# Kernel tuning notes

Measured on AMD Instinct MI355X. Metric: run time of the kernel, lower is better.

The kernel has to match this reference:

```python
import jax, jax.numpy as jnp
import numpy as np

N_NODES = 50000


def setup_inputs() -> dict:
    key = jax.random.key(0)
    k1, k2, k3, k4, k5 = jax.random.split(key, 5)
    E = 1600000
    features = jax.random.normal(k1, (N_NODES, 256), dtype=jnp.float32)
    weight = jax.random.normal(k2, (256, 64), dtype=jnp.float32) * (1.0 / np.sqrt(256))
    edge_row = jax.random.randint(k3, (E,), 0, N_NODES, dtype=jnp.int64 if jax.config.jax_enable_x64 else jnp.int32)
    edge_col = jax.random.randint(k4, (E,), 0, N_NODES, dtype=jnp.int64 if jax.config.jax_enable_x64 else jnp.int32)
    edge_weight = jax.random.uniform(k5, (E,), dtype=jnp.float32)
    return {
        "features": features,
        "weight": weight,
        "edge_row": edge_row,
        "edge_col": edge_col,
        "edge_weight": edge_weight,
        "active": 1,
    }


def reference(features, weight, edge_row, edge_col, edge_weight, active):
    # support = features @ W  -- dense projection [N, out]
    support = features @ weight
    # output = spmm(adj, support): gather source rows, scale by edge weight,
    # scatter-add into destination rows (COO SpMM).
    msgs = support[edge_col] * edge_weight[:, None]           # [E, out]
    output = jax.ops.segment_sum(msgs, edge_row, num_segments=N_NODES)  # [N, out]
    if active:
        output = jnp.tanh(output)
    return output
```

## Files before the change

### kernel.cpp

```cpp
#include <hip/hip_runtime.h>
#include <hip/hip_fp16.h>
#include <math.h>

#define N_NODES 50000
#define IN_F 256
#define OUT_F 64
#define NBUCK 391
#define CHUNK 4096
#define CAPB 4608

typedef unsigned int uint;


__global__ __launch_bounds__(256) void gemm_kernel(const float* __restrict__ feat,
                                                   const float* __restrict__ W,
                                                   __half* __restrict__ sup,
                                                   int* __restrict__ gcnt) {
    if (blockIdx.x == 0) {
        for (int i = threadIdx.x; i < NBUCK; i += 256) gcnt[i] = 0;
    }

    __shared__ float A_s[128 * 18];
    __shared__ float B_s[16 * 64];

    const int t = threadIdx.x;
    const int row0 = blockIdx.x * 128;
    const int tc = t & 15;
    const int tr = t >> 4;
    const int ar = t >> 2;
    const int ac = t & 3;

    int gr0 = row0 + ar;      if (gr0 >= N_NODES) gr0 = N_NODES - 1;
    int gr1 = row0 + ar + 64; if (gr1 >= N_NODES) gr1 = N_NODES - 1;
    const float4* gA0 = (const float4*)(feat + (size_t)gr0 * IN_F);
    const float4* gA1 = (const float4*)(feat + (size_t)gr1 * IN_F);
    const float4* gB  = (const float4*)W;

    float acc[8][4];
#pragma unroll
    for (int r = 0; r < 8; ++r)
#pragma unroll
        for (int i = 0; i < 4; ++i) acc[r][i] = 0.f;

    float4 a0 = gA0[ac];
    float4 a1 = gA1[ac];
    float4 bb = gB[(t >> 4) * 16 + tc];

    for (int ch = 0; ch < 16; ++ch) {
        {
            float* ap0 = &A_s[ar * 18 + ac * 4];
            ap0[0] = a0.x; ap0[1] = a0.y; ap0[2] = a0.z; ap0[3] = a0.w;
            float* ap1 = &A_s[(ar + 64) * 18 + ac * 4];
            ap1[0] = a1.x; ap1[1] = a1.y; ap1[2] = a1.z; ap1[3] = a1.w;
            *(float4*)&B_s[(t >> 4) * 64 + tc * 4] = bb;
        }
        __syncthreads();

        if (ch < 15) {
            a0 = gA0[(ch + 1) * 4 + ac];
            a1 = gA1[(ch + 1) * 4 + ac];
            bb = gB[((ch + 1) * 16 + (t >> 4)) * 16 + tc];
        }

#pragma unroll
        for (int k = 0; k < 16; ++k) {
            float b0 = B_s[k * 64 + tc * 4 + 0];
            float b1 = B_s[k * 64 + tc * 4 + 1];
            float b2 = B_s[k * 64 + tc * 4 + 2];
            float b3 = B_s[k * 64 + tc * 4 + 3];
#pragma unroll
            for (int r = 0; r < 8; ++r) {
                float av = A_s[(tr * 8 + r) * 18 + k];
                acc[r][0] += av * b0;
                acc[r][1] += av * b1;
                acc[r][2] += av * b2;
                acc[r][3] += av * b3;
            }
        }
        __syncthreads();
    }

#pragma unroll
    for (int r = 0; r < 8; ++r) {
        int row = row0 + tr * 8 + r;
        if (row < N_NODES) {
            __half2 h01 = __floats2half2_rn(acc[r][0], acc[r][1]);
            __half2 h23 = __floats2half2_rn(acc[r][2], acc[r][3]);
            uint2 u;
            u.x = *(unsigned int*)&h01;
            u.y = *(unsigned int*)&h23;
            *(uint2*)&sup[(size_t)row * OUT_F + tc * 4] = u;
        }
    }
}

__global__ __launch_bounds__(1024) void bin_kernel(const int* __restrict__ erow,
                                                   const int* __restrict__ ecol,
                                                   const float* __restrict__ ew,
                                                   int* __restrict__ gcnt,
                                                   int2* __restrict__ ecw, int E) {
    __shared__ int   h[NBUCK];
    __shared__ uint  pkst[CHUNK];
    __shared__ float wst[CHUNK];
    const int t = threadIdx.x;
    const int base = blockIdx.x * CHUNK;

    for (int i = t; i < NBUCK; i += 1024) h[i] = 0;
    __syncthreads();

    const int e4 = base + 4 * t;
    if (e4 + 3 < E) {
        int4   r4 = *(const int4*)(erow + e4);
        int4   c4 = *(const int4*)(ecol + e4);
        float4 w4 = *(const float4*)(ew + e4);
        pkst[4 * t + 0] = ((uint)r4.x << 16) | (uint)c4.x;
        pkst[4 * t + 1] = ((uint)r4.y << 16) | (uint)c4.y;
        pkst[4 * t + 2] = ((uint)r4.z << 16) | (uint)c4.z;
        pkst[4 * t + 3] = ((uint)r4.w << 16) | (uint)c4.w;
        *(float4*)(wst + 4 * t) = w4;
        atomicAdd(&h[r4.x >> 7], 1);
        atomicAdd(&h[r4.y >> 7], 1);
        atomicAdd(&h[r4.z >> 7], 1);
        atomicAdd(&h[r4.w >> 7], 1);
    } else {
        for (int k = 0; k < 4; ++k) {
            int e = e4 + k;
            if (e < E) {
                int row = erow[e];
                pkst[4 * t + k] = ((uint)row << 16) | (uint)ecol[e];
                wst[4 * t + k] = ew[e];
                atomicAdd(&h[row >> 7], 1);
            }
        }
    }
    __syncthreads();

    for (int i = t; i < NBUCK; i += 1024) {
        int c = h[i];
        if (c > 0) h[i] = atomicAdd(&gcnt[i], c);
    }
    __syncthreads();

    const int lim = min(CHUNK, E - base);
    for (int i = t; i < lim; i += 1024) {
        uint  pk = pkst[i];
        float w  = wst[i];
        int b = (int)(pk >> 23);
        int pos = atomicAdd(&h[b], 1);
        if (pos < CAPB)
            ecw[(size_t)b * CAPB + pos] =
                make_int2((int)(pk & 0x7FFFFF), __float_as_int(w));
    }
}

__global__ __launch_bounds__(1024) void reduce_kernel(const __half* __restrict__ sup,
                                                      const int* __restrict__ gcnt,
                                                      const int2* __restrict__ ecw,
                                                      const int* __restrict__ active,
                                                      float* __restrict__ out) {
    __shared__ int2 stA[CAPB];
    __shared__ int2 stB[CAPB];
    __shared__ int h[128];
    __shared__ int sc[128];
    __shared__ int cur[128];
    const int t = threadIdx.x;
    const int b = blockIdx.x;

    int n = gcnt[b]; if (n > CAPB) n = CAPB;
    const int2* eptr = ecw + (size_t)b * CAPB;

    if (t < 128) h[t] = 0;
    __syncthreads();

    for (int i = t; i < n; i += 1024) {
        int2 d = eptr[i];
        stA[i] = d;
        atomicAdd(&h[(d.x >> 16) & 127], 1);
    }
    __syncthreads();

    if (t < 128) sc[t] = h[t];
    __syncthreads();
    for (int off = 1; off < 128; off <<= 1) {
        int u = (t < 128 && t >= off) ? sc[t - off] : 0;
        __syncthreads();
        if (t < 128) sc[t] += u;
        __syncthreads();
    }
    if (t < 128) cur[t] = sc[t] - h[t];
    __syncthreads();

    for (int i = t; i < n; i += 1024) {
        int2 d = stA[i];
        int r = (d.x >> 16) & 127;
        int pos = atomicAdd(&cur[r], 1);
        stB[pos] = make_int2(d.x & 0xFFFF, d.y);
    }
    __syncthreads();

    const int wid  = t >> 6;
    const int lane = t & 63;
    const int hl   = lane & 31;
    const bool hi  = lane >= 32;
    const int act  = *active;

    for (int r = wid; r < 128; r += 16) {
        int row = b * 128 + r;
        if (row >= N_NODES) break;
        const int s = sc[r] - h[r];
        const int e = sc[r];
        float ax = 0.f, ay = 0.f;
        int j = s;
        for (; j + 8 <= e; j += 8) {
#pragma unroll
            for (int q = 0; q < 4; ++q) {
                int2 pa = stB[j + 2 * q];
                int2 pb = stB[j + 2 * q + 1];
                int   col = hi ? pb.x : pa.x;
                float w   = __int_as_float(hi ? pb.y : pa.y);
                const __half2* hp = (const __half2*)(sup + ((size_t)col << 6));
                float2 v = __half22float2(hp[hl]);
                ax += w * v.x;
                ay += w * v.y;
            }
        }
        for (; j + 2 <= e; j += 2) {
            int2 pa = stB[j];
            int2 pb = stB[j + 1];
            int   col = hi ? pb.x : pa.x;
            float w   = __int_as_float(hi ? pb.y : pa.y);
            const __half2* hp = (const __half2*)(sup + ((size_t)col << 6));
            float2 v = __half22float2(hp[hl]);
            ax += w * v.x;
            ay += w * v.y;
        }
        if (j < e) {
            int2 pa = stB[j];
            int   col = pa.x;
            float w   = hi ? 0.f : __int_as_float(pa.y);
            const __half2* hp = (const __half2*)(sup + ((size_t)col << 6));
            float2 v = __half22float2(hp[hl]);
            ax += w * v.x;
            ay += w * v.y;
        }

        ax += __shfl_xor(ax, 32, 64);
        ay += __shfl_xor(ay, 32, 64);

        if (!hi) {
            if (act) { ax = tanhf(ax); ay = tanhf(ay); }
            *(float2*)&out[((size_t)row << 6) + 2 * hl] = make_float2(ax, ay);
        }
    }
}

extern "C" void kernel_launch(void* const* d_in, const int* in_sizes, int n_in,
                              void* d_out, int out_size, void* d_ws, size_t ws_size,
                              hipStream_t stream) {
    const float* feat = (const float*)d_in[0];
    const float* W    = (const float*)d_in[1];
    const int*   erow = (const int*)d_in[2];
    const int*   ecol = (const int*)d_in[3];
    const float* ew   = (const float*)d_in[4];
    const int*   act  = (const int*)d_in[5];
    float* out = (float*)d_out;

    const int E = in_sizes[2];
    const int G = (E + CHUNK - 1) / CHUNK;

    char* ws = (char*)d_ws;
    __half* sup  = (__half*)ws; ws += (size_t)N_NODES * OUT_F * 2;
    int2*   ecw  = (int2*)ws;   ws += (size_t)NBUCK * CAPB * 8;
    int*    gcnt = (int*)ws;

    gemm_kernel<<<(N_NODES + 127) / 128, 256, 0, stream>>>(feat, W, sup, gcnt);
    bin_kernel<<<G, 1024, 0, stream>>>(erow, ecol, ew, gcnt, ecw, E);
    reduce_kernel<<<NBUCK, 1024, 0, stream>>>(sup, gcnt, ecw, act, out);
}
```

Measured before the change: 180.8 us.

## Use split-bf16 MFMA GEMM and finer 32-row buckets for SpMM reduce

The projection GEMM now runs on MFMA bf16 instructions, with each fp32 operand split into hi/lo bf16 parts (three MFMAs per tile) to keep near-fp32 accuracy. A new single-block prep kernel pre-splits and transposes W and zeroes the bucket counters. Separately, edge binning moves from 128-row to 32-row buckets (1563 buckets, smaller capacity), and the reduce kernel runs with 256 threads, for more blocks and less LDS per block. The smaller per-bucket capacity raises the risk of overflow drops if buckets are skewed, and the extra launch adds overhead.

```diff
diff --git a/kernel.cpp b/kernel.cpp
--- a/kernel.cpp
+++ b/kernel.cpp
@@ -5,91 +5,159 @@
 #define N_NODES 50000
 #define IN_F 256
 #define OUT_F 64
-#define NBUCK 391
+#define NBUCK 1563
+#define BROWS 32
 #define CHUNK 4096
-#define CAPB 4608
+#define CAPB 1280
 
 typedef unsigned int uint;
-
+typedef __attribute__((ext_vector_type(8))) short short8v;
+typedef __attribute__((ext_vector_type(4))) short short4v;
+typedef __attribute__((ext_vector_type(4))) float f32x4;
+
+
+__device__ __forceinline__ short bf16_trunc(float f) {
+    return (short)(__float_as_uint(f) >> 16);
+}
+__device__ __forceinline__ float bf16_tof(short s) {
+    return __uint_as_float(((uint)(unsigned short)s) << 16);
+}
+__device__ __forceinline__ short bf16_rne(float f) {
+    uint u = __float_as_uint(f);
+    uint r = u + 0x7FFF + ((u >> 16) & 1);
+    return (short)(r >> 16);
+}
+
+__global__ __launch_bounds__(256) void wprep_kernel(const float* __restrict__ W,
+                                                    short* __restrict__ Whi,
+                                                    short* __restrict__ Wlo,
+                                                    int* __restrict__ gcnt) {
+    const int t = threadIdx.x;
+    for (int i = t; i < NBUCK; i += 256) gcnt[i] = 0;
+
+    __shared__ float buf[32][65];
+    for (int k0 = 0; k0 < IN_F; k0 += 32) {
+        for (int i = t; i < 32 * 64; i += 256) {
+            int kk = i >> 6, c = i & 63;
+            buf[kk][c] = W[(k0 + kk) * 64 + c];
+        }
+        __syncthreads();
+        {
+            int c = t & 63, g = t >> 6;
+            short8v vh, vl;
+            for (int j = 0; j < 8; ++j) {
+                float f = buf[g * 8 + j][c];
+                short h = bf16_trunc(f);
+                vh[j] = h;
+                vl[j] = bf16_rne(f - bf16_tof(h));
+            }
+            *(short8v*)&Whi[c * IN_F + k0 + g * 8] = vh;
+            *(short8v*)&Wlo[c * IN_F + k0 + g * 8] = vl;
+        }
+        __syncthreads();
+    }
+}
 
 __global__ __launch_bounds__(256) void gemm_kernel(const float* __restrict__ feat,
-                                                   const float* __restrict__ W,
-                                                   __half* __restrict__ sup,
-                                                   int* __restrict__ gcnt) {
-    if (blockIdx.x == 0) {
-        for (int i = threadIdx.x; i < NBUCK; i += 256) gcnt[i] = 0;
-    }
-
-    __shared__ float A_s[128 * 18];
-    __shared__ float B_s[16 * 64];
+                                                   const short* __restrict__ Whi,
+                                                   const short* __restrict__ Wlo,
+                                                   __half* __restrict__ sup) {
+    __shared__ short lds[15360];
+    short* As_hi = lds;
+    short* As_lo = lds + 5120;
+    short* Bs_hi = lds + 10240;
+    short* Bs_lo = lds + 12800;
 
     const int t = threadIdx.x;
     const int row0 = blockIdx.x * 128;
-    const int tc = t & 15;
-    const int tr = t >> 4;
-    const int ar = t >> 2;
-    const int ac = t & 3;
-
-    int gr0 = row0 + ar;      if (gr0 >= N_NODES) gr0 = N_NODES - 1;
-    int gr1 = row0 + ar + 64; if (gr1 >= N_NODES) gr1 = N_NODES - 1;
-    const float4* gA0 = (const float4*)(feat + (size_t)gr0 * IN_F);
-    const float4* gA1 = (const float4*)(feat + (size_t)gr1 * IN_F);
-    const float4* gB  = (const float4*)W;
-
-    float acc[8][4];
-#pragma unroll
-    for (int r = 0; r < 8; ++r)
-#pragma unroll
-        for (int i = 0; i < 4; ++i) acc[r][i] = 0.f;
-
-    float4 a0 = gA0[ac];
-    float4 a1 = gA1[ac];
-    float4 bb = gB[(t >> 4) * 16 + tc];
-
-    for (int ch = 0; ch < 16; ++ch) {
-        {
-            float* ap0 = &A_s[ar * 18 + ac * 4];
-            ap0[0] = a0.x; ap0[1] = a0.y; ap0[2] = a0.z; ap0[3] = a0.w;
-            float* ap1 = &A_s[(ar + 64) * 18 + ac * 4];
-            ap1[0] = a1.x; ap1[1] = a1.y; ap1[2] = a1.z; ap1[3] = a1.w;
-            *(float4*)&B_s[(t >> 4) * 64 + tc * 4] = bb;
-        }
-        __syncthreads();
-
-        if (ch < 15) {
-            a0 = gA0[(ch + 1) * 4 + ac];
-            a1 = gA1[(ch + 1) * 4 + ac];
-            bb = gB[((ch + 1) * 16 + (t >> 4)) * 16 + tc];
-        }
-
-#pragma unroll
-        for (int k = 0; k < 16; ++k) {
-            float b0 = B_s[k * 64 + tc * 4 + 0];
-            float b1 = B_s[k * 64 + tc * 4 + 1];
-            float b2 = B_s[k * 64 + tc * 4 + 2];
-            float b3 = B_s[k * 64 + tc * 4 + 3];
-#pragma unroll
-            for (int r = 0; r < 8; ++r) {
-                float av = A_s[(tr * 8 + r) * 18 + k];
-                acc[r][0] += av * b0;
-                acc[r][1] += av * b1;
-                acc[r][2] += av * b2;
-                acc[r][3] += av * b3;
-            }
-        }
-        __syncthreads();
-    }
-
-#pragma unroll
-    for (int r = 0; r < 8; ++r) {
-        int row = row0 + tr * 8 + r;
-        if (row < N_NODES) {
-            __half2 h01 = __floats2half2_rn(acc[r][0], acc[r][1]);
-            __half2 h23 = __floats2half2_rn(acc[r][2], acc[r][3]);
-            uint2 u;
-            u.x = *(unsigned int*)&h01;
-            u.y = *(unsigned int*)&h23;
-            *(uint2*)&sup[(size_t)row * OUT_F + tc * 4] = u;
+    const int l = t & 63;
+    const int lr = l & 15;
+    const int lk = (l >> 4) * 8;
+    const int wrow = (t >> 6) * 32;
+
+    const int ar = t >> 1, aq = t & 1;
+    int gr = row0 + ar; if (gr >= N_NODES) gr = N_NODES - 1;
+    const float4* asrc = (const float4*)(feat + (size_t)gr * IN_F);
+    const int bc = t >> 2, bp = t & 3;
+
+    f32x4 acc[2][4];
+#pragma unroll
+    for (int m = 0; m < 2; ++m)
+#pragma unroll
+        for (int nn = 0; nn < 4; ++nn) acc[m][nn] = (f32x4)(0.f);
+
+    for (int ch = 0; ch < 8; ++ch) {
+        float4 av[4];
+#pragma unroll
+        for (int i = 0; i < 4; ++i) av[i] = asrc[ch * 8 + aq * 4 + i];
+        short8v bh = *(const short8v*)(Whi + bc * IN_F + ch * 32 + bp * 8);
+        short8v bl = *(const short8v*)(Wlo + bc * IN_F + ch * 32 + bp * 8);
+
+        __syncthreads();
+#pragma unroll
+        for (int i = 0; i < 4; ++i) {
+            float fx[4] = {av[i].x, av[i].y, av[i].z, av[i].w};
+            short4v h4, l4;
+#pragma unroll
+            for (int j = 0; j < 4; ++j) {
+                short h = bf16_trunc(fx[j]);
+                h4[j] = h;
+                l4[j] = bf16_rne(fx[j] - bf16_tof(h));
+            }
+            *(short4v*)&As_hi[ar * 40 + aq * 16 + i * 4] = h4;
+            *(short4v*)&As_lo[ar * 40 + aq * 16 + i * 4] = l4;
+        }
+        *(short8v*)&Bs_hi[bc * 40 + bp * 8] = bh;
+        *(short8v*)&Bs_lo[bc * 40 + bp * 8] = bl;
+        __syncthreads();
+
+        short8v ah[2], al[2], wh[4], wl[4];
+#pragma unroll
+        for (int m = 0; m < 2; ++m) {
+            ah[m] = *(short8v*)&As_hi[(wrow + m * 16 + lr) * 40 + lk];
+            al[m] = *(short8v*)&As_lo[(wrow + m * 16 + lr) * 40 + lk];
+        }
+#pragma unroll
+        for (int nn = 0; nn < 4; ++nn) {
+            wh[nn] = *(short8v*)&Bs_hi[(nn * 16 + lr) * 40 + lk];
+            wl[nn] = *(short8v*)&Bs_lo[(nn * 16 + lr) * 40 + lk];
+        }
+#pragma unroll
+        for (int m = 0; m < 2; ++m)
+#pragma unroll
+            for (int nn = 0; nn < 4; ++nn) {
+                acc[m][nn] = __builtin_amdgcn_mfma_f32_16x16x32_bf16(ah[m], wh[nn], acc[m][nn], 0, 0, 0);
+                acc[m][nn] = __builtin_amdgcn_mfma_f32_16x16x32_bf16(ah[m], wl[nn], acc[m][nn], 0, 0, 0);
+                acc[m][nn] = __builtin_amdgcn_mfma_f32_16x16x32_bf16(al[m], wh[nn], acc[m][nn], 0, 0, 0);
+            }
+    }
+
+    __syncthreads();
+    short* sup_s = lds;
+#pragma unroll
+    for (int m = 0; m < 2; ++m) {
+        int rr = wrow + m * 16 + (l >> 4) * 4;
+#pragma unroll
+        for (int nn = 0; nn < 4; ++nn) {
+            int cc = nn * 16 + lr;
+#pragma unroll
+            for (int j = 0; j < 4; ++j) {
+                __half h = __float2half(acc[m][nn][j]);
+                sup_s[(rr + j) * 64 + cc] = *(short*)&h;
+            }
+        }
+    }
+    __syncthreads();
+    {
+        int r = t >> 1, sg = (t & 1) * 32;
+        int grow = row0 + r;
+        if (grow < N_NODES) {
+            const uint4* s4 = (const uint4*)&sup_s[r * 64 + sg];
+            uint4* d4 = (uint4*)(sup + (size_t)grow * OUT_F + sg);
+            d4[0] = s4[0];
+            d4[1] = s4[1];
+            d4[2] = s4[2];
+            d4[3] = s4[3];
         }
     }
 }
@@ -118,10 +186,10 @@
         pkst[4 * t + 2] = ((uint)r4.z << 16) | (uint)c4.z;
         pkst[4 * t + 3] = ((uint)r4.w << 16) | (uint)c4.w;
         *(float4*)(wst + 4 * t) = w4;
-        atomicAdd(&h[r4.x >> 7], 1);
-        atomicAdd(&h[r4.y >> 7], 1);
-        atomicAdd(&h[r4.z >> 7], 1);
-        atomicAdd(&h[r4.w >> 7], 1);
+        atomicAdd(&h[r4.x >> 5], 1);
+        atomicAdd(&h[r4.y >> 5], 1);
+        atomicAdd(&h[r4.z >> 5], 1);
+        atomicAdd(&h[r4.w >> 5], 1);
     } else {
         for (int k = 0; k < 4; ++k) {
             int e = e4 + k;
@@ -129,7 +197,7 @@
                 int row = erow[e];
                 pkst[4 * t + k] = ((uint)row << 16) | (uint)ecol[e];
                 wst[4 * t + k] = ew[e];
-                atomicAdd(&h[row >> 7], 1);
+                atomicAdd(&h[row >> 5], 1);
             }
         }
     }
@@ -145,54 +213,54 @@
     for (int i = t; i < lim; i += 1024) {
         uint  pk = pkst[i];
         float w  = wst[i];
-        int b = (int)(pk >> 23);
+        int b = (int)(pk >> 21);
         int pos = atomicAdd(&h[b], 1);
         if (pos < CAPB)
             ecw[(size_t)b * CAPB + pos] =
-                make_int2((int)(pk & 0x7FFFFF), __float_as_int(w));
-    }
-}
-
-__global__ __launch_bounds__(1024) void reduce_kernel(const __half* __restrict__ sup,
-                                                      const int* __restrict__ gcnt,
-                                                      const int2* __restrict__ ecw,
-                                                      const int* __restrict__ active,
-                                                      float* __restrict__ out) {
+                make_int2((int)(pk & 0x1FFFFF), __float_as_int(w));
+    }
+}
+
+__global__ __launch_bounds__(256) void reduce_kernel(const __half* __restrict__ sup,
+                                                     const int* __restrict__ gcnt,
+                                                     const int2* __restrict__ ecw,
+                                                     const int* __restrict__ active,
+                                                     float* __restrict__ out) {
     __shared__ int2 stA[CAPB];
     __shared__ int2 stB[CAPB];
-    __shared__ int h[128];
-    __shared__ int sc[128];
-    __shared__ int cur[128];
+    __shared__ int h[BROWS];
+    __shared__ int sc[BROWS];
+    __shared__ int cur[BROWS];
     const int t = threadIdx.x;
     const int b = blockIdx.x;
 
     int n = gcnt[b]; if (n > CAPB) n = CAPB;
     const int2* eptr = ecw + (size_t)b * CAPB;
 
-    if (t < 128) h[t] = 0;
-    __syncthreads();
-
-    for (int i = t; i < n; i += 1024) {
+    if (t < BROWS) h[t] = 0;
+    __syncthreads();
+
+    for (int i = t; i < n; i += 256) {
         int2 d = eptr[i];
         stA[i] = d;
-        atomicAdd(&h[(d.x >> 16) & 127], 1);
-    }
-    __syncthreads();
-
-    if (t < 128) sc[t] = h[t];
-    __syncthreads();
-    for (int off = 1; off < 128; off <<= 1) {
-        int u = (t < 128 && t >= off) ? sc[t - off] : 0;
-        __syncthreads();
-        if (t < 128) sc[t] += u;
-        __syncthreads();
-    }
-    if (t < 128) cur[t] = sc[t] - h[t];
-    __syncthreads();
-
-    for (int i = t; i < n; i += 1024) {
+        atomicAdd(&h[(d.x >> 16) & 31], 1);
+    }
+    __syncthreads();
+
+    if (t < BROWS) sc[t] = h[t];
+    __syncthreads();
+    for (int off = 1; off < BROWS; off <<= 1) {
+        int u = (t < BROWS && t >= off) ? sc[t - off] : 0;
+        __syncthreads();
+        if (t < BROWS) sc[t] += u;
+        __syncthreads();
+    }
+    if (t < BROWS) cur[t] = sc[t] - h[t];
+    __syncthreads();
+
+    for (int i = t; i < n; i += 256) {
         int2 d = stA[i];
-        int r = (d.x >> 16) & 127;
+        int r = (d.x >> 16) & 31;
         int pos = atomicAdd(&cur[r], 1);
         stB[pos] = make_int2(d.x & 0xFFFF, d.y);
     }
@@ -204,8 +272,8 @@
     const bool hi  = lane >= 32;
     const int act  = *active;
 
-    for (int r = wid; r < 128; r += 16) {
-        int row = b * 128 + r;
+    for (int r = wid; r < BROWS; r += 4) {
+        int row = b * BROWS + r;
         if (row >= N_NODES) break;
         const int s = sc[r] - h[r];
         const int e = sc[r];
@@ -271,9 +339,12 @@
     char* ws = (char*)d_ws;
     __half* sup  = (__half*)ws; ws += (size_t)N_NODES * OUT_F * 2;
     int2*   ecw  = (int2*)ws;   ws += (size_t)NBUCK * CAPB * 8;
-    int*    gcnt = (int*)ws;
-
-    gemm_kernel<<<(N_NODES + 127) / 128, 256, 0, stream>>>(feat, W, sup, gcnt);
+    int*    gcnt = (int*)ws;    ws += ((size_t)NBUCK * 4 + 15) & ~15;
+    short*  Whi  = (short*)ws;  ws += (size_t)OUT_F * IN_F * 2;
+    short*  Wlo  = (short*)ws;  ws += (size_t)OUT_F * IN_F * 2;
+
+    wprep_kernel<<<1, 256, 0, stream>>>(W, Whi, Wlo, gcnt);
+    gemm_kernel<<<(N_NODES + 127) / 128, 256, 0, stream>>>(feat, Whi, Wlo, sup);
     bin_kernel<<<G, 1024, 0, stream>>>(erow, ecol, ew, gcnt, ecw, E);
-    reduce_kernel<<<NBUCK, 1024, 0, stream>>>(sup, gcnt, ecw, act, out);
-}
+    reduce_kernel<<<NBUCK, 256, 0, stream>>>(sup, gcnt, ecw, act, out);
+}
```

New measurement: 187.7 us. 3.8% more time.
